# Kernel tuning notes

Hardware: AMD Instinct MI355X
Metric: run time of the kernel (lower is better)

## Reference

```python
import math
import jax, jax.numpy as jnp
import numpy as np

B, SEQ, N_EMBD, N_HEAD, MAX_LEN = 2, 2048, 1024, 16, 2048
D_HEAD = N_EMBD // N_HEAD


def setup_inputs() -> dict:
    key = jax.random.key(0)
    k0, k1, k2, k3, k4 = jax.random.split(key, 5)
    x = jax.random.normal(k0, (B, SEQ, N_EMBD), jnp.float32)
    # nn.Linear weights stored [out_features, in_features]; scale ~ kaiming-ish
    s = 1.0 / math.sqrt(N_EMBD)
    Wq = jax.random.normal(k1, (N_EMBD, N_EMBD), jnp.float32) * s
    Wk = jax.random.normal(k2, (N_EMBD, N_EMBD), jnp.float32) * s
    Wv = jax.random.normal(k3, (N_EMBD, N_EMBD), jnp.float32) * s
    Er = jax.random.normal(k4, (MAX_LEN, D_HEAD), jnp.float32)
    return {"x": x, "Wq": Wq, "Wk": Wk, "Wv": Wv, "Er": Er}


def _skew(QEr):
    # QEr: [B, H, S, S]; mask with anti-diagonal tril-flip, then pad/reshape skew
    S = QEr.shape[-1]
    anti = jnp.flip(jnp.tril(jnp.ones((S, S), QEr.dtype)), axis=1)
    QEr = QEr * anti  # masked_fill(mask==0, 0)
    padded = jnp.pad(QEr, ((0, 0), (0, 0), (0, 0), (1, 0)))  # [B,H,S,S+1]
    Bq, H, S_, Sp1 = padded.shape
    return padded.reshape(Bq, H, Sp1, S_)[:, :, 1:, :]  # [B,H,S,S]


def reference(x, Wq, Wk, Wv, Er):
    Bx, S, E = x.shape
    H, d = N_HEAD, D_HEAD

    def proj(W):
        return jnp.einsum('bse,fe->bsf', x, W).reshape(Bx, S, H, d).transpose(0, 2, 1, 3)

    q, k, v = proj(Wq), proj(Wk), proj(Wv)  # [B,H,S,d]
    qk = jnp.einsum('bhqd,bhkd->bhqk', q, k)
    Er_s = Er[MAX_LEN - S:, :]  # [S, d]
    QEr = jnp.einsum('bhqd,rd->bhqr', q, Er_s)  # [B,H,S,S]
    Srel = _skew(QEr)
    attn = (qk + Srel) / math.sqrt(d)
    causal = jnp.tril(jnp.ones((S, S), bool))
    attn = jnp.where(causal, attn, -jnp.inf)
    p = jax.nn.softmax(attn, axis=-1)
    out = jnp.einsum('bhqk,bhkd->bhqd', p, v)
    return out.transpose(0, 2, 1, 3).reshape(Bx, S, E)
```

## Files before the change

### kernel.cpp

```cpp
#include <hip/hip_runtime.h>
#include <hip/hip_bf16.h>
#include <stdint.h>

#define S_LEN 2048
#define EMB   1024
#define NH    16
#define DH    64
#define BATCH 2

typedef short bf16x8 __attribute__((ext_vector_type(8)));
typedef short bf16x4 __attribute__((ext_vector_type(4)));
typedef float f32x4  __attribute__((ext_vector_type(4)));

__device__ __forceinline__ unsigned short f2bf(float f) {
    union { float f; unsigned int u; } v; v.f = f;
    unsigned int r = v.u + 0x7FFFu + ((v.u >> 16) & 1u);
    return (unsigned short)(r >> 16);
}

__device__ __forceinline__ short f2bf_fast(float f) {
    __hip_bfloat16 h = __float2bfloat16(f);
    return *reinterpret_cast<short*>(&h);
}

__device__ __forceinline__ float bf2f(short s) {
    union { unsigned int u; float f; } v;
    v.u = ((unsigned int)(unsigned short)s) << 16;
    return v.f;
}

__device__ __forceinline__ bf16x8 load8f_to_bf(const float* __restrict__ p) {
    const float4* p4 = (const float4*)p;
    float4 x0 = p4[0];
    float4 x1 = p4[1];
    bf16x8 r;
    r[0] = (short)f2bf(x0.x); r[1] = (short)f2bf(x0.y);
    r[2] = (short)f2bf(x0.z); r[3] = (short)f2bf(x0.w);
    r[4] = (short)f2bf(x1.x); r[5] = (short)f2bf(x1.y);
    r[6] = (short)f2bf(x1.z); r[7] = (short)f2bf(x1.w);
    return r;
}

__device__ __forceinline__ void bar_lds() {
    asm volatile("s_waitcnt lgkmcnt(0)" ::: "memory");
    __builtin_amdgcn_sched_barrier(0);
    __builtin_amdgcn_s_barrier();
    __builtin_amdgcn_sched_barrier(0);
}

__device__ __forceinline__ void fence_lds() {
    asm volatile("s_waitcnt lgkmcnt(0)" ::: "memory");
    __builtin_amdgcn_sched_barrier(0);
}

__device__ __forceinline__ void gload_lds16(const unsigned short* g, unsigned short* l) {
    __builtin_amdgcn_global_load_lds(
        (const __attribute__((address_space(1))) unsigned int*)g,
        (__attribute__((address_space(3))) unsigned int*)l, 16, 0, 0);
}

__global__ __launch_bounds__(256) void cvt_bf16(
    const float* __restrict__ x,  const float* __restrict__ wq,
    const float* __restrict__ wk, const float* __restrict__ wv,
    const float* __restrict__ er,
    unsigned short* __restrict__ xb, unsigned short* __restrict__ wb,
    unsigned short* __restrict__ erb)
{
    const int NX = 4194304 / 8, NW = 1048576 / 8, NE = 131072 / 8;
    const int total = NX + 3 * NW + NE;
    for (int i8 = blockIdx.x * 256 + threadIdx.x; i8 < total; i8 += gridDim.x * 256) {
        const float* src; unsigned short* dst; int off;
        if      (i8 < NX)          { src = x;  dst = xb;            off = i8; }
        else if (i8 < NX + NW)     { src = wq; dst = wb;            off = i8 - NX; }
        else if (i8 < NX + 2 * NW) { src = wk; dst = wb + 1048576;  off = i8 - NX - NW; }
        else if (i8 < NX + 3 * NW) { src = wv; dst = wb + 2097152;  off = i8 - NX - 2 * NW; }
        else                       { src = er; dst = erb;           off = i8 - NX - 3 * NW; }
        ((bf16x8*)dst)[off] = load8f_to_bf(src + (size_t)off * 8);
    }
}

__global__ __launch_bounds__(256) void proj_kernel_bf(
    const unsigned short* __restrict__ xb, const unsigned short* __restrict__ wb,
    unsigned short* __restrict__ Qb, unsigned short* __restrict__ Kb,
    unsigned short* __restrict__ Vt)
{
    __shared__ __align__(16) unsigned short Al[128 * 64];
    __shared__ __align__(16) unsigned short Bl[128 * 64];

    const int tid  = threadIdx.x;
    const int lane = tid & 63;
    const int w    = tid >> 6;
    const int wr   = w >> 1;
    const int wc   = w & 1;
    const int m0   = blockIdx.x * 128;
    const int c0   = blockIdx.y * 128;
    const int wsel = c0 >> 10;
    const int f0   = c0 & 1023;
    const unsigned short* __restrict__ W = wb + (size_t)wsel * 1048576;

    const int lr = lane & 15;
    const int g  = lane >> 4;

    const int srow8 = tid >> 3;
    const int scol  = (((tid & 7) ^ (srow8 & 7))) * 8;

    f32x4 acc[4][4];
#pragma unroll
    for (int i = 0; i < 4; i++)
#pragma unroll
        for (int n = 0; n < 4; n++) acc[i][n] = (f32x4){0.f, 0.f, 0.f, 0.f};

    for (int k0 = 0; k0 < 1024; k0 += 64) {
        __syncthreads();
#pragma unroll
        for (int i = 0; i < 4; i++) {
            gload_lds16(&xb[(size_t)(m0 + i * 32 + srow8) * 1024 + k0 + scol],
                        &Al[(i * 4 + w) * 512]);
            gload_lds16(&W [(size_t)(f0 + i * 32 + srow8) * 1024 + k0 + scol],
                        &Bl[(i * 4 + w) * 512]);
        }
        __syncthreads();

#pragma unroll
        for (int kk = 0; kk < 2; kk++) {
            bf16x8 a[4], b[4];
#pragma unroll
            for (int i = 0; i < 4; i++) {
                int ar = wr * 64 + i * 16 + lr;
                a[i] = *(const bf16x8*)&Al[ar * 64 + (((kk * 4 + g) ^ (ar & 7)) * 8)];
            }
#pragma unroll
            for (int n = 0; n < 4; n++) {
                int br = wc * 64 + n * 16 + lr;
                b[n] = *(const bf16x8*)&Bl[br * 64 + (((kk * 4 + g) ^ (br & 7)) * 8)];
            }
#pragma unroll
            for (int i = 0; i < 4; i++)
#pragma unroll
                for (int n = 0; n < 4; n++)
                    acc[i][n] = __builtin_amdgcn_mfma_f32_16x16x32_bf16(a[i], b[n], acc[i][n], 0, 0, 0);
        }
    }

#pragma unroll
    for (int i = 0; i < 4; i++) {
#pragma unroll
        for (int n = 0; n < 4; n++) {
#pragma unroll
            for (int j = 0; j < 4; j++) {
                int row_m = m0 + wr * 64 + i * 16 + g * 4 + j;
                int c     = c0 + wc * 64 + n * 16 + lr;
                int f     = c & 1023;
                int h     = f >> 6;
                int dd    = f & 63;
                int bb    = row_m >> 11;
                int s     = row_m & 2047;
                int bh    = bb * 16 + h;
                unsigned short bv = f2bf(acc[i][n][j]);
                if (wsel == 0)      Qb[((size_t)bh * 2048 + s) * 64 + dd] = bv;
                else if (wsel == 1) Kb[((size_t)bh * 2048 + s) * 64 + dd] = bv;
                else                Vt[((size_t)bh * 64 + dd) * 2048 + s] = bv;
            }
        }
    }
}

__global__ __launch_bounds__(256) void proj_kernel_f32(
    const float* __restrict__ x,
    const float* __restrict__ Wq, const float* __restrict__ Wk,
    const float* __restrict__ Wv,
    unsigned short* __restrict__ Qb, unsigned short* __restrict__ Kb,
    unsigned short* __restrict__ Vt)
{
    const int tid  = threadIdx.x;
    const int lane = tid & 63;
    const int w    = tid >> 6;
    const int wr   = w >> 1;
    const int wc   = w & 1;
    const int m0   = blockIdx.x * 128 + wr * 64;
    const int c0   = blockIdx.y * 128 + wc * 64;
    const int wsel = c0 >> 10;
    const int f0   = c0 & 1023;
    const float* __restrict__ W = (wsel == 0) ? Wq : (wsel == 1) ? Wk : Wv;

    const int lr = lane & 15;
    const int lk = (lane >> 4) * 8;

    f32x4 acc[4][4];
#pragma unroll
    for (int i = 0; i < 4; i++)
#pragma unroll
        for (int n = 0; n < 4; n++) acc[i][n] = (f32x4){0.f, 0.f, 0.f, 0.f};

    for (int k0 = 0; k0 < 1024; k0 += 32) {
        bf16x8 a[4], b[4];
#pragma unroll
        for (int i = 0; i < 4; i++)
            a[i] = load8f_to_bf(&x[(size_t)(m0 + i * 16 + lr) * 1024 + k0 + lk]);
#pragma unroll
        for (int n = 0; n < 4; n++)
            b[n] = load8f_to_bf(&W[(size_t)(f0 + n * 16 + lr) * 1024 + k0 + lk]);
#pragma unroll
        for (int i = 0; i < 4; i++)
#pragma unroll
            for (int n = 0; n < 4; n++)
                acc[i][n] = __builtin_amdgcn_mfma_f32_16x16x32_bf16(a[i], b[n], acc[i][n], 0, 0, 0);
    }

    const int g = lane >> 4;
#pragma unroll
    for (int i = 0; i < 4; i++) {
#pragma unroll
        for (int n = 0; n < 4; n++) {
#pragma unroll
            for (int j = 0; j < 4; j++) {
                int row_m = m0 + i * 16 + g * 4 + j;
                int c     = c0 + n * 16 + lr;
                int f     = c & 1023;
                int h     = f >> 6;
                int dd    = f & 63;
                int bb    = row_m >> 11;
                int s     = row_m & 2047;
                int bh    = bb * 16 + h;
                unsigned short bv = f2bf(acc[i][n][j]);
                if (wsel == 0)      Qb[((size_t)bh * 2048 + s) * 64 + dd] = bv;
                else if (wsel == 1) Kb[((size_t)bh * 2048 + s) * 64 + dd] = bv;
                else                Vt[((size_t)bh * 64 + dd) * 2048 + s] = bv;
            }
        }
    }
}

__global__ void cvt_er(const float* __restrict__ Er, unsigned short* __restrict__ Erb, int n)
{
    int i = blockIdx.x * 256 + threadIdx.x;
    if (i < n) Erb[i] = f2bf(Er[i]);
}

__global__ __launch_bounds__(256) void attn_kernel(
    const unsigned short* __restrict__ Qb, const unsigned short* __restrict__ Kb,
    const unsigned short* __restrict__ Vt, const unsigned short* __restrict__ Erb,
    float* __restrict__ out)
{
    __shared__ __align__(16) unsigned short Kl[2][64 * 64];
    __shared__ __align__(16) unsigned short Vl[2][64 * 68];
    __shared__ __align__(16) unsigned short El[192 * 64];
    __shared__ __align__(16) float          Rt[4][80][18];

    const int tid  = threadIdx.x;
    const int lane = tid & 63;
    const int w    = tid >> 6;

    const int i0  = blockIdx.x;
    const int xcd = i0 & 7;
    const int b2  = (i0 >> 3) & 3;
    const int qt  = 31 - (i0 >> 5);
    const int bh  = (xcd << 2) | b2;

    const int lr = lane & 15;
    const int g  = lane >> 4;
    const int lk = g * 8;

    const unsigned short* __restrict__ Qrow = Qb + (size_t)bh * 2048 * 64;
    const unsigned short* __restrict__ Krow = Kb + (size_t)bh * 2048 * 64;
    const unsigned short* __restrict__ Vrow = Vt + (size_t)bh * 64 * 2048;

    const float SCL = 0.125f * 1.44269504089f;
    const int bb  = bh >> 4;
    const int h   = bh & 15;
    const int q0  = qt * 64;
    const int q0w = q0 + w * 16;
    const int eoff = 48 - 16 * w;
    const int rbT0 = 1984 - q0;

    bf16x8 aq[2];
#pragma unroll
    for (int kk = 0; kk < 2; kk++) {
        bf16x8 q = *(const bf16x8*)&Qrow[(size_t)(q0w + lr) * 64 + kk * 32 + lk];
#pragma unroll
        for (int e = 0; e < 8; e++)
            q[e] = f2bf_fast(bf2f(q[e]) * SCL);
        aq[kk] = q;
    }

    f32x4 o[4];
#pragma unroll
    for (int m = 0; m < 4; m++) o[m] = (f32x4){0.f, 0.f, 0.f, 0.f};
    float lsum = 0.f;

    bf16x8 sk[2], sv[2], se[4];
    const int o8u = (tid & 7) * 8;

    auto kv_load = [&](int kt) {
        const int k0 = kt * 64;
#pragma unroll
        for (int i = 0; i < 2; i++) {
            int kr = ((i * 256 + tid) >> 3);
            sk[i] = *(const bf16x8*)&Krow[(size_t)(k0 + kr) * 64 + o8u];
        }
#pragma unroll
        for (int i = 0; i < 2; i++) {
            int d = ((i * 256 + tid) >> 3);
            sv[i] = *(const bf16x8*)&Vrow[(size_t)d * 2048 + k0 + o8u];
        }
    };
    auto kv_write = [&](int p) {
#pragma unroll
        for (int i = 0; i < 2; i++) {
            int kr = ((i * 256 + tid) >> 3);
            *(bf16x8*)&Kl[p][(kr * 64 + o8u) ^ ((kr & 7) << 3)] = sk[i];
        }
#pragma unroll
        for (int i = 0; i < 2; i++) {
            int d = ((i * 256 + tid) >> 3);
            *(bf16x8*)&Vl[p][d * 68 + o8u] = sv[i];
        }
    };
    auto e_load4 = [&](int base) {
#pragma unroll
        for (int i = 0; i < 4; i++) {
            int r = base + ((i * 256 + tid) >> 3);
            int rr = r > 2047 ? 2047 : r;
            se[i] = *(const bf16x8*)&Erb[(size_t)rr * 64 + o8u];
        }
    };
    auto e_load2 = [&](int base) {
#pragma unroll
        for (int i = 0; i < 2; i++) {
            int r = base + ((i * 256 + tid) >> 3);
            int rr = r > 2047 ? 2047 : r;
            se[i] = *(const bf16x8*)&Erb[(size_t)rr * 64 + o8u];
        }
    };
    auto e_write4 = [&](int bslot) {
#pragma unroll
        for (int i = 0; i < 4; i++) {
            int slot = bslot + ((i * 256 + tid) >> 3);
            if (slot >= 192) slot -= 192;
            *(bf16x8*)&El[(slot * 64 + o8u) ^ ((slot & 7) << 3)] = se[i];
        }
    };
    auto e_write2 = [&](int bslot) {
#pragma unroll
        for (int i = 0; i < 2; i++) {
            int slot = bslot + ((i * 256 + tid) >> 3);
            if (slot >= 192) slot -= 192;
            *(bf16x8*)&El[(slot * 64 + o8u) ^ ((slot & 7) << 3)] = se[i];
        }
    };

    int eb = rbT0 % 192;
    kv_load(0);
    e_load4(rbT0);
    kv_write(0);
    e_write4(eb);

#pragma unroll 1
    for (int kt = 0; kt <= qt; ++kt) {
        bar_lds();

        if (kt < qt) {
            kv_load(kt + 1);
            e_load2(rbT0 + 64 * kt + 128);
        }

        const int p = kt & 1;

        f32x4 s[4], r[5];
#pragma unroll
        for (int n = 0; n < 4; n++) s[n] = (f32x4){0.f, 0.f, 0.f, 0.f};
#pragma unroll
        for (int n = 0; n < 5; n++) r[n] = (f32x4){0.f, 0.f, 0.f, 0.f};
        __builtin_amdgcn_s_setprio(1);
#pragma unroll
        for (int kk = 0; kk < 2; kk++) {
            bf16x8 kb[4], be[5];
#pragma unroll
            for (int n = 0; n < 4; n++) {
                int kr = n * 16 + lr;
                kb[n] = *(const bf16x8*)&Kl[p][(kr * 64 + kk * 32 + lk) ^ ((kr & 7) << 3)];
            }
#pragma unroll
            for (int n = 0; n < 5; n++) {
                int slot = eb + eoff + n * 16 + lr;
                if (slot >= 192) slot -= 192;
                be[n] = *(const bf16x8*)&El[(slot * 64 + kk * 32 + lk) ^ ((slot & 7) << 3)];
            }
#pragma unroll
            for (int n = 0; n < 4; n++)
                s[n] = __builtin_amdgcn_mfma_f32_16x16x32_bf16(kb[n], aq[kk], s[n], 0, 0, 0);
#pragma unroll
            for (int n = 0; n < 5; n++)
                r[n] = __builtin_amdgcn_mfma_f32_16x16x32_bf16(be[n], aq[kk], r[n], 0, 0, 0);
        }
        __builtin_amdgcn_s_setprio(0);

#pragma unroll
        for (int n = 0; n < 5; n++)
#pragma unroll
            for (int j = 0; j < 4; j++)
                Rt[w][n * 16 + g * 4 + j][lr] = r[n][j];

        fence_lds();

        float rs = 0.f;
        bf16x4 pa[4];
        if (kt != qt) {
#pragma unroll
            for (int n = 0; n < 4; n++)
#pragma unroll
                for (int j = 0; j < 4; j++) {
                    int kl = n * 16 + g * 4 + j;
                    float pv = exp2f(s[n][j] + Rt[w][kl + 15 - lr][lr]);
                    rs += pv;
                    pa[n][j] = f2bf_fast(pv);
                }
        } else {
#pragma unroll
            for (int n = 0; n < 4; n++)
#pragma unroll
                for (int j = 0; j < 4; j++) {
                    int kl = n * 16 + g * 4 + j;
                    float sc = s[n][j] + Rt[w][kl + 15 - lr][lr];
                    if (kl > w * 16 + lr) sc = -1e30f;
                    float pv = exp2f(sc);
                    rs += pv;
                    pa[n][j] = f2bf_fast(pv);
                }
        }
        lsum += rs;

        __builtin_amdgcn_s_setprio(1);
#pragma unroll
        for (int m = 0; m < 4; m++) {
#pragma unroll
            for (int n = 0; n < 4; n++) {
                int d = 16 * m + lr;
                bf16x4 vb = *(const bf16x4*)&Vl[p][d * 68 + 16 * n + 4 * g];
                o[m] = __builtin_amdgcn_mfma_f32_16x16x16bf16_1k(pa[n], vb, o[m], 0, 0, 0);
            }
        }
        __builtin_amdgcn_s_setprio(0);

        if (kt < qt) {
            kv_write(p ^ 1);
            int wslot = eb + 128;
            if (wslot >= 192) wslot -= 192;
            e_write2(wslot);
        }
        eb += 64;
        if (eb >= 192) eb -= 192;
    }

    float ls = lsum;
    ls += __shfl_xor(ls, 16);
    ls += __shfl_xor(ls, 32);
    float linv = 1.0f / ls;
#pragma unroll
    for (int j = 0; j < 4; j++) {
        float lj = __shfl(linv, g * 4 + j);
#pragma unroll
        for (int m = 0; m < 4; m++) {
            int row = q0w + g * 4 + j;
            int col = h * 64 + 16 * m + lr;
            out[((size_t)bb * 2048 + row) * 1024 + col] = o[m][j] * lj;
        }
    }
}

extern "C" void kernel_launch(void* const* d_in, const int* in_sizes, int n_in,
                              void* d_out, int out_size, void* d_ws, size_t ws_size,
                              hipStream_t stream)
{
    const float* x  = (const float*)d_in[0];
    const float* Wq = (const float*)d_in[1];
    const float* Wk = (const float*)d_in[2];
    const float* Wv = (const float*)d_in[3];
    const float* Er = (const float*)d_in[4];
    float* out = (float*)d_out;

    char* ws = (char*)d_ws;
    const size_t MB = 1024 * 1024;
    unsigned short* Qb  = (unsigned short*)(ws);
    unsigned short* Kb  = (unsigned short*)(ws + 8  * MB);
    unsigned short* Vt  = (unsigned short*)(ws + 16 * MB);
    unsigned short* Erb = (unsigned short*)(ws + 24 * MB);
    unsigned short* xb  = (unsigned short*)(ws + 25 * MB);
    unsigned short* wb  = (unsigned short*)(ws + 33 * MB);

    if (ws_size >= (size_t)39 * MB) {
        cvt_bf16<<<dim3(1024), dim3(256), 0, stream>>>(x, Wq, Wk, Wv, Er, xb, wb, Erb);
        proj_kernel_bf<<<dim3(32, 24), dim3(256), 0, stream>>>(xb, wb, Qb, Kb, Vt);
    } else {
        cvt_er<<<dim3(512), dim3(256), 0, stream>>>(Er, Erb, 2048 * 64);
        proj_kernel_f32<<<dim3(32, 24), dim3(256), 0, stream>>>(x, Wq, Wk, Wv, Qb, Kb, Vt);
    }
    attn_kernel<<<dim3(1024), dim3(256), 0, stream>>>(Qb, Kb, Vt, Erb, out);
}
```

Baseline: 128.3 us.

## Process 128-row query tiles per block so each wave reuses K/V/Er tiles for two subtiles

Each block now handles 128 query rows instead of 64, with each wave computing two 16-row subtiles that share the same K, V and Er LDS tiles and the V fragments held in registers. The grid is halved to 512 blocks, the Er ring buffer grows to 256 slots with cheaper power-of-two wraparound, and the relative-score transpose scratch is stored in bf16 to save LDS. The aim is to cut global/LDS traffic and loop overhead per query row, at the cost of more register pressure, fewer blocks, worse load balance across the causal triangle, and extra rounding of the relative term.

```diff
diff --git a/kernel.cpp b/kernel.cpp
--- a/kernel.cpp
+++ b/kernel.cpp
@@ -23,9 +23,9 @@
     return *reinterpret_cast<short*>(&h);
 }
 
-__device__ __forceinline__ float bf2f(short s) {
+__device__ __forceinline__ float bf2f(unsigned short s) {
     union { unsigned int u; float f; } v;
-    v.u = ((unsigned int)(unsigned short)s) << 16;
+    v.u = ((unsigned int)s) << 16;
     return v.f;
 }
 
@@ -244,8 +244,8 @@
 {
     __shared__ __align__(16) unsigned short Kl[2][64 * 64];
     __shared__ __align__(16) unsigned short Vl[2][64 * 68];
-    __shared__ __align__(16) unsigned short El[192 * 64];
-    __shared__ __align__(16) float          Rt[4][80][18];
+    __shared__ __align__(16) unsigned short El[256 * 64];
+    __shared__ __align__(16) unsigned short Rt[4][80 * 18];
 
     const int tid  = threadIdx.x;
     const int lane = tid & 63;
@@ -254,7 +254,7 @@
     const int i0  = blockIdx.x;
     const int xcd = i0 & 7;
     const int b2  = (i0 >> 3) & 3;
-    const int qt  = 31 - (i0 >> 5);
+    const int qt  = 15 - (i0 >> 5);
     const int bh  = (xcd << 2) | b2;
 
     const int lr = lane & 15;
@@ -268,25 +268,31 @@
     const float SCL = 0.125f * 1.44269504089f;
     const int bb  = bh >> 4;
     const int h   = bh & 15;
-    const int q0  = qt * 64;
-    const int q0w = q0 + w * 16;
-    const int eoff = 48 - 16 * w;
-    const int rbT0 = 1984 - q0;
-
-    bf16x8 aq[2];
-#pragma unroll
-    for (int kk = 0; kk < 2; kk++) {
-        bf16x8 q = *(const bf16x8*)&Qrow[(size_t)(q0w + lr) * 64 + kk * 32 + lk];
-#pragma unroll
-        for (int e = 0; e < 8; e++)
-            q[e] = f2bf_fast(bf2f(q[e]) * SCL);
-        aq[kk] = q;
-    }
-
-    f32x4 o[4];
-#pragma unroll
-    for (int m = 0; m < 4; m++) o[m] = (f32x4){0.f, 0.f, 0.f, 0.f};
-    float lsum = 0.f;
+    const int q0  = qt * 128;
+    const int qs0 = q0 + 32 * w;
+    const int qs1 = qs0 + 16;
+    const int ktmax = 2 * qt + 1;
+    const int rbT0  = 1920 - q0;
+    const int beB   = 96 - 32 * w;
+    unsigned short* __restrict__ RtW = &Rt[w][0];
+
+    bf16x8 aq[2][2];
+#pragma unroll
+    for (int s = 0; s < 2; s++)
+#pragma unroll
+        for (int kk = 0; kk < 2; kk++) {
+            int qs = s ? qs1 : qs0;
+            bf16x8 q = *(const bf16x8*)&Qrow[(size_t)(qs + lr) * 64 + kk * 32 + lk];
+#pragma unroll
+            for (int e = 0; e < 8; e++)
+                q[e] = f2bf_fast(bf2f((unsigned short)q[e]) * SCL);
+            aq[s][kk] = q;
+        }
+
+    f32x4 o0[4], o1[4];
+#pragma unroll
+    for (int m = 0; m < 4; m++) { o0[m] = (f32x4){0.f,0.f,0.f,0.f}; o1[m] = (f32x4){0.f,0.f,0.f,0.f}; }
+    float lsum0 = 0.f, lsum1 = 0.f;
 
     bf16x8 sk[2], sv[2], se[4];
     const int o8u = (tid & 7) * 8;
@@ -335,135 +341,200 @@
     auto e_write4 = [&](int bslot) {
 #pragma unroll
         for (int i = 0; i < 4; i++) {
-            int slot = bslot + ((i * 256 + tid) >> 3);
-            if (slot >= 192) slot -= 192;
+            int slot = (bslot + ((i * 256 + tid) >> 3)) & 255;
             *(bf16x8*)&El[(slot * 64 + o8u) ^ ((slot & 7) << 3)] = se[i];
         }
     };
     auto e_write2 = [&](int bslot) {
 #pragma unroll
         for (int i = 0; i < 2; i++) {
-            int slot = bslot + ((i * 256 + tid) >> 3);
-            if (slot >= 192) slot -= 192;
+            int slot = (bslot + ((i * 256 + tid) >> 3)) & 255;
             *(bf16x8*)&El[(slot * 64 + o8u) ^ ((slot & 7) << 3)] = se[i];
         }
     };
 
-    int eb = rbT0 % 192;
+    int ecs = ((30 - 2 * qt) & 3) * 64;
     kv_load(0);
+    kv_write(0);
     e_load4(rbT0);
-    kv_write(0);
-    e_write4(eb);
+    e_write4(ecs);
+    e_load2(rbT0 + 128);
+    e_write2((ecs + 128) & 255);
 
 #pragma unroll 1
-    for (int kt = 0; kt <= qt; ++kt) {
+    for (int kt = 0; kt <= ktmax; ++kt) {
+        const int k0 = kt * 64;
         bar_lds();
 
-        if (kt < qt) {
+        if (kt < ktmax) {
             kv_load(kt + 1);
-            e_load2(rbT0 + 64 * kt + 128);
+            e_load2(rbT0 + 64 * kt + 192);
         }
 
         const int p = kt & 1;
 
-        f32x4 s[4], r[5];
-#pragma unroll
-        for (int n = 0; n < 4; n++) s[n] = (f32x4){0.f, 0.f, 0.f, 0.f};
-#pragma unroll
-        for (int n = 0; n < 5; n++) r[n] = (f32x4){0.f, 0.f, 0.f, 0.f};
+        f32x4 s0[4], s1[4], r0[5], r1[5];
+#pragma unroll
+        for (int n = 0; n < 4; n++) { s0[n] = (f32x4){0.f,0.f,0.f,0.f}; s1[n] = (f32x4){0.f,0.f,0.f,0.f}; }
+#pragma unroll
+        for (int n = 0; n < 5; n++) { r0[n] = (f32x4){0.f,0.f,0.f,0.f}; r1[n] = (f32x4){0.f,0.f,0.f,0.f}; }
         __builtin_amdgcn_s_setprio(1);
 #pragma unroll
         for (int kk = 0; kk < 2; kk++) {
-            bf16x8 kb[4], be[5];
+            bf16x8 kb[4], be[6];
 #pragma unroll
             for (int n = 0; n < 4; n++) {
                 int kr = n * 16 + lr;
                 kb[n] = *(const bf16x8*)&Kl[p][(kr * 64 + kk * 32 + lk) ^ ((kr & 7) << 3)];
             }
 #pragma unroll
+            for (int n = 0; n < 6; n++) {
+                int slot = (ecs + beB + n * 16 + lr) & 255;
+                be[n] = *(const bf16x8*)&El[(slot * 64 + kk * 32 + lk) ^ ((slot & 7) << 3)];
+            }
+#pragma unroll
+            for (int n = 0; n < 4; n++) {
+                s0[n] = __builtin_amdgcn_mfma_f32_16x16x32_bf16(kb[n], aq[0][kk], s0[n], 0, 0, 0);
+                s1[n] = __builtin_amdgcn_mfma_f32_16x16x32_bf16(kb[n], aq[1][kk], s1[n], 0, 0, 0);
+            }
+#pragma unroll
             for (int n = 0; n < 5; n++) {
-                int slot = eb + eoff + n * 16 + lr;
-                if (slot >= 192) slot -= 192;
-                be[n] = *(const bf16x8*)&El[(slot * 64 + kk * 32 + lk) ^ ((slot & 7) << 3)];
-            }
-#pragma unroll
-            for (int n = 0; n < 4; n++)
-                s[n] = __builtin_amdgcn_mfma_f32_16x16x32_bf16(kb[n], aq[kk], s[n], 0, 0, 0);
-#pragma unroll
-            for (int n = 0; n < 5; n++)
-                r[n] = __builtin_amdgcn_mfma_f32_16x16x32_bf16(be[n], aq[kk], r[n], 0, 0, 0);
+                r0[n] = __builtin_amdgcn_mfma_f32_16x16x32_bf16(be[n + 1], aq[0][kk], r0[n], 0, 0, 0);
+                r1[n] = __builtin_amdgcn_mfma_f32_16x16x32_bf16(be[n],     aq[1][kk], r1[n], 0, 0, 0);
+            }
         }
         __builtin_amdgcn_s_setprio(0);
 
-#pragma unroll
-        for (int n = 0; n < 5; n++)
-#pragma unroll
-            for (int j = 0; j < 4; j++)
-                Rt[w][n * 16 + g * 4 + j][lr] = r[n][j];
-
-        fence_lds();
-
-        float rs = 0.f;
-        bf16x4 pa[4];
-        if (kt != qt) {
-#pragma unroll
-            for (int n = 0; n < 4; n++)
-#pragma unroll
-                for (int j = 0; j < 4; j++) {
-                    int kl = n * 16 + g * 4 + j;
-                    float pv = exp2f(s[n][j] + Rt[w][kl + 15 - lr][lr]);
-                    rs += pv;
-                    pa[n][j] = f2bf_fast(pv);
-                }
-        } else {
-#pragma unroll
-            for (int n = 0; n < 4; n++)
-#pragma unroll
-                for (int j = 0; j < 4; j++) {
-                    int kl = n * 16 + g * 4 + j;
-                    float sc = s[n][j] + Rt[w][kl + 15 - lr][lr];
-                    if (kl > w * 16 + lr) sc = -1e30f;
-                    float pv = exp2f(sc);
-                    rs += pv;
-                    pa[n][j] = f2bf_fast(pv);
-                }
-        }
-        lsum += rs;
-
-        __builtin_amdgcn_s_setprio(1);
-#pragma unroll
-        for (int m = 0; m < 4; m++) {
+        bf16x4 vb[4][4];
+#pragma unroll
+        for (int m = 0; m < 4; m++)
 #pragma unroll
             for (int n = 0; n < 4; n++) {
                 int d = 16 * m + lr;
-                bf16x4 vb = *(const bf16x4*)&Vl[p][d * 68 + 16 * n + 4 * g];
-                o[m] = __builtin_amdgcn_mfma_f32_16x16x16bf16_1k(pa[n], vb, o[m], 0, 0, 0);
-            }
-        }
-        __builtin_amdgcn_s_setprio(0);
-
-        if (kt < qt) {
+                vb[m][n] = *(const bf16x4*)&Vl[p][d * 68 + 16 * n + 4 * g];
+            }
+
+        if (k0 <= qs0 + 15) {
+#pragma unroll
+            for (int n = 0; n < 5; n++)
+#pragma unroll
+                for (int j = 0; j < 4; j++)
+                    RtW[(n * 16 + g * 4 + j) * 18 + lr] = (unsigned short)f2bf_fast(r0[n][j]);
+            fence_lds();
+            float rs = 0.f;
+            bf16x4 pa[4];
+            if (k0 + 63 <= qs0) {
+#pragma unroll
+                for (int n = 0; n < 4; n++)
+#pragma unroll
+                    for (int j = 0; j < 4; j++) {
+                        int kl = n * 16 + g * 4 + j;
+                        float pv = exp2f(s0[n][j] + bf2f(RtW[(kl + 15 - lr) * 18 + lr]));
+                        rs += pv;
+                        pa[n][j] = f2bf_fast(pv);
+                    }
+            } else {
+#pragma unroll
+                for (int n = 0; n < 4; n++)
+#pragma unroll
+                    for (int j = 0; j < 4; j++) {
+                        int kl = n * 16 + g * 4 + j;
+                        float sc = s0[n][j] + bf2f(RtW[(kl + 15 - lr) * 18 + lr]);
+                        if (k0 + kl > qs0 + lr) sc = -1e30f;
+                        float pv = exp2f(sc);
+                        rs += pv;
+                        pa[n][j] = f2bf_fast(pv);
+                    }
+            }
+            lsum0 += rs;
+            __builtin_amdgcn_s_setprio(1);
+#pragma unroll
+            for (int m = 0; m < 4; m++)
+#pragma unroll
+                for (int n = 0; n < 4; n++)
+                    o0[m] = __builtin_amdgcn_mfma_f32_16x16x16bf16_1k(pa[n], vb[m][n], o0[m], 0, 0, 0);
+            __builtin_amdgcn_s_setprio(0);
+        }
+
+        if (k0 <= qs1 + 15) {
+#pragma unroll
+            for (int n = 0; n < 5; n++)
+#pragma unroll
+                for (int j = 0; j < 4; j++)
+                    RtW[(n * 16 + g * 4 + j) * 18 + lr] = (unsigned short)f2bf_fast(r1[n][j]);
+            fence_lds();
+            float rs = 0.f;
+            bf16x4 pa[4];
+            if (k0 + 63 <= qs1) {
+#pragma unroll
+                for (int n = 0; n < 4; n++)
+#pragma unroll
+                    for (int j = 0; j < 4; j++) {
+                        int kl = n * 16 + g * 4 + j;
+                        float pv = exp2f(s1[n][j] + bf2f(RtW[(kl + 15 - lr) * 18 + lr]));
+                        rs += pv;
+                        pa[n][j] = f2bf_fast(pv);
+                    }
+            } else {
+#pragma unroll
+                for (int n = 0; n < 4; n++)
+#pragma unroll
+                    for (int j = 0; j < 4; j++) {
+                        int kl = n * 16 + g * 4 + j;
+                        float sc = s1[n][j] + bf2f(RtW[(kl + 15 - lr) * 18 + lr]);
+                        if (k0 + kl > qs1 + lr) sc = -1e30f;
+                        float pv = exp2f(sc);
+                        rs += pv;
+                        pa[n][j] = f2bf_fast(pv);
+                    }
+            }
+            lsum1 += rs;
+            __builtin_amdgcn_s_setprio(1);
+#pragma unroll
+            for (int m = 0; m < 4; m++)
+#pragma unroll
+                for (int n = 0; n < 4; n++)
+                    o1[m] = __builtin_amdgcn_mfma_f32_16x16x16bf16_1k(pa[n], vb[m][n], o1[m], 0, 0, 0);
+            __builtin_amdgcn_s_setprio(0);
+        }
+
+        if (kt < ktmax) {
             kv_write(p ^ 1);
-            int wslot = eb + 128;
-            if (wslot >= 192) wslot -= 192;
-            e_write2(wslot);
-        }
-        eb += 64;
-        if (eb >= 192) eb -= 192;
-    }
-
-    float ls = lsum;
-    ls += __shfl_xor(ls, 16);
-    ls += __shfl_xor(ls, 32);
-    float linv = 1.0f / ls;
-#pragma unroll
-    for (int j = 0; j < 4; j++) {
-        float lj = __shfl(linv, g * 4 + j);
-#pragma unroll
-        for (int m = 0; m < 4; m++) {
-            int row = q0w + g * 4 + j;
-            int col = h * 64 + 16 * m + lr;
-            out[((size_t)bb * 2048 + row) * 1024 + col] = o[m][j] * lj;
+            e_write2((ecs + 192) & 255);
+        }
+        ecs = (ecs + 64) & 255;
+    }
+
+    {
+        float ls = lsum0;
+        ls += __shfl_xor(ls, 16);
+        ls += __shfl_xor(ls, 32);
+        float linv = 1.0f / ls;
+#pragma unroll
+        for (int j = 0; j < 4; j++) {
+            float lj = __shfl(linv, g * 4 + j);
+#pragma unroll
+            for (int m = 0; m < 4; m++) {
+                int row = qs0 + g * 4 + j;
+                int col = h * 64 + 16 * m + lr;
+                out[((size_t)bb * 2048 + row) * 1024 + col] = o0[m][j] * lj;
+            }
+        }
+    }
+    {
+        float ls = lsum1;
+        ls += __shfl_xor(ls, 16);
+        ls += __shfl_xor(ls, 32);
+        float linv = 1.0f / ls;
+#pragma unroll
+        for (int j = 0; j < 4; j++) {
+            float lj = __shfl(linv, g * 4 + j);
+#pragma unroll
+            for (int m = 0; m < 4; m++) {
+                int row = qs1 + g * 4 + j;
+                int col = h * 64 + 16 * m + lr;
+                out[((size_t)bb * 2048 + row) * 1024 + col] = o1[m][j] * lj;
+            }
         }
     }
 }
@@ -495,5 +566,5 @@
         cvt_er<<<dim3(512), dim3(256), 0, stream>>>(Er, Erb, 2048 * 64);
         proj_kernel_f32<<<dim3(32, 24), dim3(256), 0, stream>>>(x, Wq, Wk, Wv, Qb, Kb, Vt);
     }
-    attn_kernel<<<dim3(1024), dim3(256), 0, stream>>>(Qb, Kb, Vt, Erb, out);
-}
+    attn_kernel<<<dim3(512), dim3(256), 0, stream>>>(Qb, Kb, Vt, Erb, out);
+}
```

Result: slower. 155.1 us (+20.8%).
